# Performance work log

Measured on AMD Instinct MI355X. Metric: run time of the kernel, lower is better.

## Reference

```python
import jax, jax.numpy as jnp
import numpy as np

H = 16  # n_heads
MAX_LEN = 1024


def _skew(x):
    # x: (B, H, N, M) with M == N. Pad 1 column on the left, reshape, drop first row.
    B, h, N, M = x.shape
    x = jnp.pad(x, ((0, 0), (0, 0), (0, 0), (1, 0)))  # (B,H,N,M+1)
    x = x.reshape(B, h, M + 1, N)
    return x[:, :, 1:, :]  # (B,H,N,N)


def setup_inputs() -> dict:
    key = jax.random.key(0)
    ks = jax.random.split(key, 10)
    B, N, C, T = 8, 1024, 1024, 256
    s = 0.02
    return {
        "x": jax.random.normal(ks[0], (B, N, C), dtype=jnp.float32),
        "time_emb": jax.random.normal(ks[1], (B, T), dtype=jnp.float32),
        "W_qkv": jax.random.normal(ks[2], (C, 3 * C), dtype=jnp.float32) * s,
        "b_qkv": jnp.zeros((3 * C,), dtype=jnp.float32),
        "W_time": jax.random.normal(ks[3], (T, 3 * C), dtype=jnp.float32) * s,
        "b_time": jnp.zeros((3 * C,), dtype=jnp.float32),
        "W_out": jax.random.normal(ks[4], (C, C), dtype=jnp.float32) * s,
        "b_out": jnp.zeros((C,), dtype=jnp.float32),
        "Er": jax.random.normal(ks[5], (MAX_LEN, C // H), dtype=jnp.float32) * s,
    }


def reference(x, time_emb, W_qkv, b_qkv, W_time, b_time, W_out, b_out, Er):
    B, N, C = x.shape
    D = C // H
    # token qkv: (B,N,3C) -> (3,B,H,N,D)
    qkv = (x @ W_qkv + b_qkv).reshape(B, N, 3, H, D).transpose(2, 0, 3, 1, 4)
    q, k, v = qkv[0], qkv[1], qkv[2]
    # time qkv: (B,3C) -> (3,B,H,1,D)
    tqkv = (time_emb @ W_time + b_time).reshape(B, 1, 3, H, D).transpose(2, 0, 3, 1, 4)
    q = q + tqkv[0]
    k = k + tqkv[1]
    v = v + tqkv[2]
    # relative position bias
    Er_sl = Er[Er.shape[0] - N:]                      # (N, D)
    rel = jnp.einsum('bhnd,md->bhnm', q, Er_sl)        # (B,H,N,N)
    rel = _skew(rel)
    scale = D ** (-0.5)
    scores = jnp.einsum('bhnd,bhmd->bhnm', q, k) * scale + rel
    attn = jax.nn.softmax(scores, axis=-1)
    out = jnp.einsum('bhnm,bhmd->bhnd', attn, v)       # (B,H,N,D)
    out = out.transpose(0, 2, 1, 3).reshape(B, N, C)
    return out @ W_out + b_out
```

## Files before the change

### kernel.cpp

```cpp
#include <hip/hip_runtime.h>
#include <math.h>

typedef __attribute__((ext_vector_type(8))) short short8;
typedef __attribute__((ext_vector_type(8))) unsigned short ushort8;
typedef __attribute__((ext_vector_type(4))) unsigned short us4;
typedef __attribute__((ext_vector_type(4))) unsigned int u32x4;
typedef __attribute__((ext_vector_type(4))) float f32x4;

#define NH 16
#define HD 64
#define SEQ 1024
#define NB 8
#define CH 1024
#define TD 256
#define GROW 1025
#define LOG2E 1.4426950408889634f

__device__ __forceinline__ unsigned short f2bf(float f) {
  union { float f; unsigned int u; } v; v.f = f;
  unsigned int r = v.u + 0x7FFFu + ((v.u >> 16) & 1u);
  return (unsigned short)(r >> 16);
}
__device__ __forceinline__ float bf2f(unsigned short s) {
  union { unsigned int u; float f; } v; v.u = ((unsigned int)s) << 16;
  return v.f;
}
__device__ __forceinline__ float hexp2(float x) {
  float r;
  asm("v_exp_f32 %0, %1" : "=v"(r) : "v"(x));
  return r;
}
__device__ __forceinline__ void gload_lds16(const unsigned short* g, unsigned short* l) {
  __builtin_amdgcn_global_load_lds(
      (const __attribute__((address_space(1))) unsigned int*)g,
      (__attribute__((address_space(3))) unsigned int*)l, 16, 0, 0);
}

__global__ __launch_bounds__(256) void time_proj_kernel(
    const float* __restrict__ time_emb, const float* __restrict__ W_time,
    const float* __restrict__ b_time, float* __restrict__ tqkv) {
  int idx = blockIdx.x * 256 + threadIdx.x;
  if (idx >= NB * 3072) return;
  int b = idx / 3072, c = idx % 3072;
  float s = b_time[c];
  for (int t = 0; t < TD; ++t) s += time_emb[b * TD + t] * W_time[t * 3072 + c];
  tqkv[idx] = s;
}

__global__ __launch_bounds__(256) void er_convert_kernel(
    const float* __restrict__ Er, unsigned short* __restrict__ Er_bf) {
  int i = blockIdx.x * 256 + threadIdx.x;
  if (i < SEQ * HD) Er_bf[i] = f2bf(Er[i] * LOG2E);
}

__global__ __launch_bounds__(256) void convert_bf_kernel(
    const float* __restrict__ in, unsigned short* __restrict__ out, int n8) {
  int i = blockIdx.x * 256 + threadIdx.x;
  if (i >= n8) return;
  float4 a = ((const float4*)in)[2 * i];
  float4 b = ((const float4*)in)[2 * i + 1];
  ushort8 o;
  o[0] = f2bf(a.x); o[1] = f2bf(a.y); o[2] = f2bf(a.z); o[3] = f2bf(a.w);
  o[4] = f2bf(b.x); o[5] = f2bf(b.y); o[6] = f2bf(b.z); o[7] = f2bf(b.w);
  ((ushort8*)out)[i] = o;
}

__global__ __launch_bounds__(256) void transpose_bf_kernel(
    const float* __restrict__ W, unsigned short* __restrict__ Wt, int R, int Cc) {
  __shared__ float T[64][65];
  int r0 = blockIdx.y * 64, c0 = blockIdx.x * 64;
  for (int idx = threadIdx.x; idx < 4096; idx += 256) {
    int r = idx >> 6, c = idx & 63;
    T[r][c] = W[(size_t)(r0 + r) * Cc + c0 + c];
  }
  __syncthreads();
  for (int idx = threadIdx.x; idx < 4096; idx += 256) {
    int c = idx >> 6, r = idx & 63;
    Wt[(size_t)(c0 + c) * R + r0 + r] = f2bf(T[r][c]);
  }
}

__global__ __launch_bounds__(256) void qkv_gemm_mfma(
    const unsigned short* __restrict__ A, const unsigned short* __restrict__ Bt,
    const float* __restrict__ bqkv, const float* __restrict__ tqkv,
    unsigned short* __restrict__ qb, unsigned short* __restrict__ ksw,
    unsigned short* __restrict__ vtsw) {
  __shared__ unsigned short As[128 * 32];
  __shared__ unsigned short Bs[128 * 32];
  const int m0 = blockIdx.x * 128, n0 = blockIdx.y * 128;
  const int tid = threadIdx.x, l = tid & 63, w = tid >> 6;
  const int wm = w >> 1, wn = w & 1;
  const int grp = l >> 4, col = l & 15;
  f32x4 acc[4][4];
#pragma unroll
  for (int mi = 0; mi < 4; ++mi)
#pragma unroll
    for (int ni = 0; ni < 4; ++ni) acc[mi][ni] = (f32x4){0.f, 0.f, 0.f, 0.f};

  for (int k0 = 0; k0 < 1024; k0 += 32) {
    __syncthreads();
#pragma unroll
    for (int i = 0; i < 2; ++i) {
      int seg = i * 256 + w * 64 + l;
      int mr = seg >> 2, kq = seg & 3;
      gload_lds16(A + (size_t)(m0 + mr) * 1024 + k0 + kq * 8,
                  &As[(i * 256 + w * 64) * 8]);
      gload_lds16(Bt + (size_t)(n0 + mr) * 1024 + k0 + kq * 8,
                  &Bs[(i * 256 + w * 64) * 8]);
    }
    __syncthreads();
    short8 af[4], bfv[4];
#pragma unroll
    for (int mi = 0; mi < 4; ++mi)
      af[mi] = *(const short8*)&As[(wm * 64 + mi * 16 + col) * 32 + grp * 8];
#pragma unroll
    for (int ni = 0; ni < 4; ++ni)
      bfv[ni] = *(const short8*)&Bs[(wn * 64 + ni * 16 + col) * 32 + grp * 8];
#pragma unroll
    for (int mi = 0; mi < 4; ++mi)
#pragma unroll
      for (int ni = 0; ni < 4; ++ni)
        acc[mi][ni] = __builtin_amdgcn_mfma_f32_16x16x32_bf16(af[mi], bfv[ni], acc[mi][ni], 0, 0, 0);
  }

  const int bidx = m0 >> 10;
  const int which = n0 >> 10;
  float biasv[4];
  int hhv[4], dv[4];
#pragma unroll
  for (int ni = 0; ni < 4; ++ni) {
    int c = n0 + wn * 64 + ni * 16 + col;
    biasv[ni] = bqkv[c] + tqkv[bidx * 3072 + c];
    int cc = c & 1023;
    hhv[ni] = cc >> 6;
    dv[ni] = cc & 63;
  }
  if (which == 2) {
    int t = (m0 & 1023) + wm * 64;
#pragma unroll
    for (int ni = 0; ni < 4; ++ni) {
      size_t rowb = ((size_t)(bidx * 16 + hhv[ni]) * 64 + dv[ni]) * 1024;
      int swz = (dv[ni] & 7) << 3;
#pragma unroll
      for (int rr = 0; rr < 4; ++rr) {
        int kbase = (grp * 4 + rr) * 4;
        int colix = t + ((kbase & ~7) ^ swz) + (kbase & 7);
        us4 pk;
#pragma unroll
        for (int mi = 0; mi < 4; ++mi) pk[mi] = f2bf(acc[mi][ni][rr] + biasv[ni]);
        *(us4*)&vtsw[rowb + colix] = pk;
      }
    }
  } else if (which == 1) {
#pragma unroll
    for (int mi = 0; mi < 4; ++mi)
#pragma unroll
      for (int rr = 0; rr < 4; ++rr) {
        int nn = (m0 + wm * 64 + mi * 16 + grp * 4 + rr) & 1023;
#pragma unroll
        for (int ni = 0; ni < 4; ++ni) {
          size_t bhh = (size_t)(bidx * 16 + hhv[ni]);
          ksw[(bhh * 1024 + nn) * 64 + (dv[ni] ^ ((nn & 7) << 3))] =
              f2bf(acc[mi][ni][rr] + biasv[ni]);
        }
      }
  } else {
#pragma unroll
    for (int mi = 0; mi < 4; ++mi)
#pragma unroll
      for (int rr = 0; rr < 4; ++rr) {
        int nn = (m0 + wm * 64 + mi * 16 + grp * 4 + rr) & 1023;
#pragma unroll
        for (int ni = 0; ni < 4; ++ni) {
          size_t bhh = (size_t)(bidx * 16 + hhv[ni]);
          qb[(bhh * 1024 + nn) * 64 + dv[ni]] = f2bf(acc[mi][ni][rr] + biasv[ni]);
        }
      }
  }
}

__global__ __launch_bounds__(256) void out_gemm_mfma(
    const unsigned short* __restrict__ A, const unsigned short* __restrict__ Bt,
    const float* __restrict__ bias, float* __restrict__ out) {
  __shared__ unsigned short As[128 * 32];
  __shared__ unsigned short Bs[128 * 32];
  const int m0 = blockIdx.x * 128, n0 = blockIdx.y * 128;
  const int tid = threadIdx.x, l = tid & 63, w = tid >> 6;
  const int wm = w >> 1, wn = w & 1;
  const int grp = l >> 4, col = l & 15;
  f32x4 acc[4][4];
#pragma unroll
  for (int mi = 0; mi < 4; ++mi)
#pragma unroll
    for (int ni = 0; ni < 4; ++ni) acc[mi][ni] = (f32x4){0.f, 0.f, 0.f, 0.f};

  for (int k0 = 0; k0 < 1024; k0 += 32) {
    __syncthreads();
#pragma unroll
    for (int i = 0; i < 2; ++i) {
      int seg = i * 256 + w * 64 + l;
      int mr = seg >> 2, kq = seg & 3;
      gload_lds16(A + (size_t)(m0 + mr) * 1024 + k0 + kq * 8,
                  &As[(i * 256 + w * 64) * 8]);
      gload_lds16(Bt + (size_t)(n0 + mr) * 1024 + k0 + kq * 8,
                  &Bs[(i * 256 + w * 64) * 8]);
    }
    __syncthreads();
    short8 af[4], bfv[4];
#pragma unroll
    for (int mi = 0; mi < 4; ++mi)
      af[mi] = *(const short8*)&As[(wm * 64 + mi * 16 + col) * 32 + grp * 8];
#pragma unroll
    for (int ni = 0; ni < 4; ++ni)
      bfv[ni] = *(const short8*)&Bs[(wn * 64 + ni * 16 + col) * 32 + grp * 8];
#pragma unroll
    for (int mi = 0; mi < 4; ++mi)
#pragma unroll
      for (int ni = 0; ni < 4; ++ni)
        acc[mi][ni] = __builtin_amdgcn_mfma_f32_16x16x32_bf16(af[mi], bfv[ni], acc[mi][ni], 0, 0, 0);
  }
  float bv[4];
#pragma unroll
  for (int ni = 0; ni < 4; ++ni) bv[ni] = bias[n0 + wn * 64 + ni * 16 + col];
#pragma unroll
  for (int mi = 0; mi < 4; ++mi)
#pragma unroll
    for (int rr = 0; rr < 4; ++rr) {
      int row = m0 + wm * 64 + mi * 16 + grp * 4 + rr;
#pragma unroll
      for (int ni = 0; ni < 4; ++ni) {
        int c = n0 + wn * 64 + ni * 16 + col;
        out[(size_t)row * 1024 + c] = acc[mi][ni][rr] + bv[ni];
      }
    }
}

__global__ __launch_bounds__(256) void g_gemm2(
    const unsigned short* __restrict__ qb, int bh_base,
    const unsigned short* __restrict__ Er_bf,
    unsigned short* __restrict__ Gp) {
  const int n0 = blockIdx.x * 64;
  const int jq = blockIdx.y;
  const int bhl = blockIdx.z;
  const int bh = bh_base + bhl;
  const int tid = threadIdx.x, l = tid & 63, w = tid >> 6;
  const int grp = l >> 4, col = l & 15;
  const int jw = jq * 256 + w * 64;

  short8 aq[4][2];
#pragma unroll
  for (int rf = 0; rf < 4; ++rf)
#pragma unroll
    for (int dc = 0; dc < 2; ++dc)
      aq[rf][dc] = *(const short8*)(qb + ((size_t)bh * SEQ + n0 + rf * 16 + col) * HD + dc * 32 + grp * 8);

  f32x4 acc[4][4];
#pragma unroll
  for (int rf = 0; rf < 4; ++rf)
#pragma unroll
    for (int cf = 0; cf < 4; ++cf) acc[rf][cf] = (f32x4){0.f, 0.f, 0.f, 0.f};

#pragma unroll
  for (int cf = 0; cf < 4; ++cf)
#pragma unroll
    for (int dc = 0; dc < 2; ++dc) {
      short8 bfrag = *(const short8*)(Er_bf + (size_t)(jw + cf * 16 + col) * HD + dc * 32 + grp * 8);
#pragma unroll
      for (int rf = 0; rf < 4; ++rf)
        acc[rf][cf] = __builtin_amdgcn_mfma_f32_16x16x32_bf16(aq[rf][dc], bfrag, acc[rf][cf], 0, 0, 0);
    }

#pragma unroll
  for (int rf = 0; rf < 4; ++rf)
#pragma unroll
    for (int cf = 0; cf < 4; ++cf)
#pragma unroll
      for (int rr = 0; rr < 4; ++rr) {
        int n = n0 + rf * 16 + grp * 4 + rr;
        int j = jw + cf * 16 + col;
        Gp[((size_t)(bhl * SEQ + n)) * GROW + j] = f2bf(acc[rf][cf][rr]);
      }
  if (jq == 3 && tid < 64) {
    int n = n0 + tid;
    Gp[((size_t)(bhl * SEQ + n)) * GROW + 1024] = 0;
  }
}

__global__ __launch_bounds__(256) void attn_kernel(
    const unsigned short* __restrict__ qb, const unsigned short* __restrict__ ksw,
    const unsigned short* __restrict__ vtsw, const unsigned short* __restrict__ Gp,
    unsigned short* __restrict__ attn_o, int bh_base) {
  __shared__ __align__(16) unsigned short KsL[2][4096];
  __shared__ __align__(16) unsigned short VtL[2][4096];
  __shared__ __align__(16) unsigned short Band[2][64][72];
  __shared__ __align__(16) unsigned short Pw[4][16][72];

  const int wg = blockIdx.x + 16 * blockIdx.y;
  const int chunk = 2 * gridDim.y;
  const int nid = (wg & 7) * chunk + (wg >> 3);
  const int bhl = nid >> 4;
  const int n0 = (nid & 15) * 64;
  const int bh = bh_base + bhl;
  const int b = bh >> 4, h = bh & 15;
  const int tid = threadIdx.x, lane = tid & 63, wq = tid >> 6;
  const int grp = lane >> 4, col = lane & 15;
  const int n0w = n0 + wq * 16;

  short8 aq[2];
#pragma unroll
  for (int dc = 0; dc < 2; ++dc)
    aq[dc] = *(const short8*)(qb + ((size_t)(bh * SEQ + n0w + col)) * HD + dc * 32 + grp * 8);

  f32x4 acco[4];
#pragma unroll
  for (int oc = 0; oc < 4; ++oc) acco[oc] = (f32x4){0.f, 0.f, 0.f, 0.f};
  float mrun = -INFINITY, lrun = 0.f;

  const float scale2 = 0.125f * LOG2E;
  const unsigned short* kbh = ksw + (size_t)bh * SEQ * HD;
  const unsigned short* vbh = vtsw + (size_t)bh * HD * SEQ;
  const unsigned short* gbase = Gp + (size_t)(bhl * SEQ + n0) * GROW + (1016 - n0);

  auto STAGE = [&](int buf, int m0) {
#pragma unroll
    for (int i = 0; i < 2; ++i) {
      int gi = i * 256 + wq * 64 + lane;
      int row = gi >> 3, gc = gi & 7;
      gload_lds16(kbh + (((size_t)(m0 + row)) << 6) + gc * 8,
                  &KsL[buf][(i * 256 + wq * 64) * 8]);
      gload_lds16(vbh + (((size_t)row) << 10) + m0 + gc * 8,
                  &VtL[buf][(i * 256 + wq * 64) * 8]);
    }
    const unsigned short* gsrc = gbase + m0;
    unsigned short* bdst = &Band[buf][0][0];
    const int g0 = wq * 144;
#pragma unroll
    for (int it = 0; it < 2; ++it) {
      int g = g0 + it * 64 + lane;
      int r = g / 9, seg = g - r * 9;
      gload_lds16(gsrc + r * 1024 + seg * 8, bdst + g * 8);
    }
    if (lane < 16) {
      int g = g0 + 128 + lane;
      int r = g / 9, seg = g - r * 9;
      gload_lds16(gsrc + r * 1024 + seg * 8, bdst + g * 8);
    }
  };

  STAGE(0, 0);
  __syncthreads();

  for (int t = 0; t < 16; ++t) {
    const int cur = t & 1;
    if (t < 15) STAGE(cur ^ 1, (t + 1) * 64);
    f32x4 acc[4];
#pragma unroll
    for (int mc = 0; mc < 4; ++mc) acc[mc] = (f32x4){0.f, 0.f, 0.f, 0.f};
    __builtin_amdgcn_s_setprio(1);
#pragma unroll
    for (int mc = 0; mc < 4; ++mc)
#pragma unroll
      for (int dc = 0; dc < 2; ++dc) {
        short8 bk = *(const short8*)&KsL[cur][(mc * 16 + col) * 64 + (((dc * 4 + grp) ^ (col & 7)) << 3)];
        acc[mc] = __builtin_amdgcn_mfma_f32_16x16x32_bf16(bk, aq[dc], acc[mc], 0, 0, 0);
      }
    __builtin_amdgcn_s_setprio(0);
    float s[4][4];
    const int dr = wq * 16 + col;
#pragma unroll
    for (int mc = 0; mc < 4; ++mc)
#pragma unroll
      for (int r = 0; r < 4; ++r)
        s[mc][r] = fmaf(acc[mc][r], scale2, bf2f(Band[cur][dr][7 + mc * 16 + grp * 4 + r]));
    float mx = s[0][0];
#pragma unroll
    for (int mc = 0; mc < 4; ++mc)
#pragma unroll
      for (int r = 0; r < 4; ++r) mx = fmaxf(mx, s[mc][r]);
    mx = fmaxf(mx, __shfl_xor(mx, 16));
    mx = fmaxf(mx, __shfl_xor(mx, 32));
    if (mx > mrun) {
      float cr = hexp2(mrun - mx);
      mrun = mx;
      lrun *= cr;
#pragma unroll
      for (int oc = 0; oc < 4; ++oc)
#pragma unroll
        for (int r = 0; r < 4; ++r) acco[oc][r] *= cr;
    }
    float p[4][4];
#pragma unroll
    for (int mc = 0; mc < 4; ++mc)
#pragma unroll
      for (int r = 0; r < 4; ++r) {
        p[mc][r] = hexp2(s[mc][r] - mrun);
        lrun += p[mc][r];
      }
    unsigned int wpk[8];
#pragma unroll
    for (int r = 0; r < 4; ++r)
#pragma unroll
      for (int mh = 0; mh < 2; ++mh)
        asm("v_cvt_pk_bf16_f32 %0, %1, %2"
            : "=v"(wpk[r * 2 + mh]) : "v"(p[mh * 2][r]), "v"(p[mh * 2 + 1][r]));
    *(u32x4*)&Pw[wq][col][grp * 16] = (u32x4){wpk[0], wpk[1], wpk[2], wpk[3]};
    *(u32x4*)&Pw[wq][col][grp * 16 + 8] = (u32x4){wpk[4], wpk[5], wpk[6], wpk[7]};
    short8 ap[2];
#pragma unroll
    for (int kc = 0; kc < 2; ++kc)
      ap[kc] = *(const short8*)&Pw[wq][col][kc * 32 + grp * 8];
    __builtin_amdgcn_s_setprio(1);
#pragma unroll
    for (int oc = 0; oc < 4; ++oc)
#pragma unroll
      for (int kc = 0; kc < 2; ++kc) {
        short8 bv = *(const short8*)&VtL[cur][(oc * 16 + col) * 64 + (((kc * 4 + grp) ^ (col & 7)) << 3)];
        acco[oc] = __builtin_amdgcn_mfma_f32_16x16x32_bf16(bv, ap[kc], acco[oc], 0, 0, 0);
      }
    __builtin_amdgcn_s_setprio(0);
    __syncthreads();
  }
  float tot = lrun;
  tot += __shfl_xor(tot, 16);
  tot += __shfl_xor(tot, 32);
  float inv = 1.0f / tot;
  const int n = n0w + col;
#pragma unroll
  for (int oc = 0; oc < 4; ++oc) {
    us4 pk;
#pragma unroll
    for (int r = 0; r < 4; ++r) pk[r] = f2bf(acco[oc][r] * inv);
    *(us4*)&attn_o[((size_t)(b * SEQ + n)) * CH + h * HD + oc * 16 + grp * 4] = pk;
  }
}

extern "C" void kernel_launch(void* const* d_in, const int* in_sizes, int n_in,
                              void* d_out, int out_size, void* d_ws, size_t ws_size,
                              hipStream_t stream) {
  const float* x        = (const float*)d_in[0];
  const float* time_emb = (const float*)d_in[1];
  const float* W_qkv    = (const float*)d_in[2];
  const float* b_qkv    = (const float*)d_in[3];
  const float* W_time   = (const float*)d_in[4];
  const float* b_time   = (const float*)d_in[5];
  const float* W_out    = (const float*)d_in[6];
  const float* b_out    = (const float*)d_in[7];
  const float* Er       = (const float*)d_in[8];
  float* out = (float*)d_out;

  char* p = (char*)d_ws;
  float* tqkv = (float*)p;                      p += 98304;
  unsigned short* qb = (unsigned short*)p;      p += 16777216;
  unsigned short* ksw = (unsigned short*)p;     p += 16777216;
  unsigned short* vtsw = (unsigned short*)p;    p += 16777216;
  unsigned short* attn_o = (unsigned short*)p;  p += 16777216;
  unsigned short* Er_bf = (unsigned short*)p;   p += 131072;
  unsigned short* Wout_t = (unsigned short*)p;  p += 2097152;
  unsigned short* x_bf = (unsigned short*)p;
  unsigned short* Wqkv_t = x_bf + (size_t)8388608;
  unsigned short* Gp = (unsigned short*)p;

  size_t fixed = (size_t)(p - (char*)d_ws);
  int slab_bh = (ws_size >= fixed + (size_t)64 * 2099200) ? 64 : 32;
  int nslab = 128 / slab_bh;

  er_convert_kernel<<<256, 256, 0, stream>>>(Er, Er_bf);
  time_proj_kernel<<<96, 256, 0, stream>>>(time_emb, W_time, b_time, tqkv);
  convert_bf_kernel<<<4096, 256, 0, stream>>>(x, x_bf, 1048576);
  transpose_bf_kernel<<<dim3(48, 16), 256, 0, stream>>>(W_qkv, Wqkv_t, 1024, 3072);
  transpose_bf_kernel<<<dim3(16, 16), 256, 0, stream>>>(W_out, Wout_t, 1024, 1024);
  qkv_gemm_mfma<<<dim3(64, 24), 256, 0, stream>>>(x_bf, Wqkv_t, b_qkv, tqkv, qb, ksw, vtsw);
  for (int s = 0; s < nslab; ++s) {
    int bh_base = s * slab_bh;
    g_gemm2<<<dim3(16, 4, slab_bh), 256, 0, stream>>>(qb, bh_base, Er_bf, Gp);
    attn_kernel<<<dim3(16, slab_bh), 256, 0, stream>>>(qb, ksw, vtsw, Gp, attn_o, bh_base);
  }
  out_gemm_mfma<<<dim3(64, 8), 256, 0, stream>>>(attn_o, Wout_t, b_out, out);
}
```

Before: 383.9 us.

## Double attention query tile per block and split QKV GEMM into per-output templated launches

The attention kernel now handles 128 query rows per block, with each wave owning two 16-row fragments. Every K/V fragment loaded from LDS therefore feeds two MFMAs, which halves K/V staging traffic per query. The band buffer is now single-buffered at twice the size and is restaged after a mid-iteration barrier. This adds registers and a sync per step and halves the grid size. Separately, the QKV GEMM is split into three template-specialized launches so the Q/K/V epilogue branch is resolved at compile time.

```diff
diff --git a/kernel.cpp b/kernel.cpp
--- a/kernel.cpp
+++ b/kernel.cpp
@@ -80,11 +80,11 @@
   }
 }
 
-__global__ __launch_bounds__(256) void qkv_gemm_mfma(
+template <int WHICH>
+__global__ __launch_bounds__(256) void qkv_gemm_w(
     const unsigned short* __restrict__ A, const unsigned short* __restrict__ Bt,
-    const float* __restrict__ bqkv, const float* __restrict__ tqkv,
-    unsigned short* __restrict__ qb, unsigned short* __restrict__ ksw,
-    unsigned short* __restrict__ vtsw) {
+    const float* __restrict__ bq, const float* __restrict__ tq,
+    unsigned short* __restrict__ dst) {
   __shared__ unsigned short As[128 * 32];
   __shared__ unsigned short Bs[128 * 32];
   const int m0 = blockIdx.x * 128, n0 = blockIdx.y * 128;
@@ -124,18 +124,16 @@
   }
 
   const int bidx = m0 >> 10;
-  const int which = n0 >> 10;
   float biasv[4];
   int hhv[4], dv[4];
 #pragma unroll
   for (int ni = 0; ni < 4; ++ni) {
-    int c = n0 + wn * 64 + ni * 16 + col;
-    biasv[ni] = bqkv[c] + tqkv[bidx * 3072 + c];
-    int cc = c & 1023;
-    hhv[ni] = cc >> 6;
-    dv[ni] = cc & 63;
-  }
-  if (which == 2) {
+    int c2 = n0 + wn * 64 + ni * 16 + col;
+    biasv[ni] = bq[c2] + tq[bidx * 3072 + c2];
+    hhv[ni] = c2 >> 6;
+    dv[ni] = c2 & 63;
+  }
+  if (WHICH == 2) {
     int t = (m0 & 1023) + wm * 64;
 #pragma unroll
     for (int ni = 0; ni < 4; ++ni) {
@@ -148,10 +146,10 @@
         us4 pk;
 #pragma unroll
         for (int mi = 0; mi < 4; ++mi) pk[mi] = f2bf(acc[mi][ni][rr] + biasv[ni]);
-        *(us4*)&vtsw[rowb + colix] = pk;
-      }
-    }
-  } else if (which == 1) {
+        *(us4*)&dst[rowb + colix] = pk;
+      }
+    }
+  } else if (WHICH == 1) {
 #pragma unroll
     for (int mi = 0; mi < 4; ++mi)
 #pragma unroll
@@ -160,7 +158,7 @@
 #pragma unroll
         for (int ni = 0; ni < 4; ++ni) {
           size_t bhh = (size_t)(bidx * 16 + hhv[ni]);
-          ksw[(bhh * 1024 + nn) * 64 + (dv[ni] ^ ((nn & 7) << 3))] =
+          dst[(bhh * 1024 + nn) * 64 + (dv[ni] ^ ((nn & 7) << 3))] =
               f2bf(acc[mi][ni][rr] + biasv[ni]);
         }
       }
@@ -173,7 +171,7 @@
 #pragma unroll
         for (int ni = 0; ni < 4; ++ni) {
           size_t bhh = (size_t)(bidx * 16 + hhv[ni]);
-          qb[(bhh * 1024 + nn) * 64 + dv[ni]] = f2bf(acc[mi][ni][rr] + biasv[ni]);
+          dst[(bhh * 1024 + nn) * 64 + dv[ni]] = f2bf(acc[mi][ni][rr] + biasv[ni]);
         }
       }
   }
@@ -292,36 +290,39 @@
     unsigned short* __restrict__ attn_o, int bh_base) {
   __shared__ __align__(16) unsigned short KsL[2][4096];
   __shared__ __align__(16) unsigned short VtL[2][4096];
-  __shared__ __align__(16) unsigned short Band[2][64][72];
-  __shared__ __align__(16) unsigned short Pw[4][16][72];
-
-  const int wg = blockIdx.x + 16 * blockIdx.y;
-  const int chunk = 2 * gridDim.y;
+  __shared__ __align__(16) unsigned short Band[128][72];
+  __shared__ __align__(16) unsigned short Pw[4][32][72];
+
+  const int wg = blockIdx.x + 8 * blockIdx.y;
+  const int chunk = gridDim.y;
   const int nid = (wg & 7) * chunk + (wg >> 3);
-  const int bhl = nid >> 4;
-  const int n0 = (nid & 15) * 64;
+  const int bhl = nid >> 3;
+  const int n0 = (nid & 7) * 128;
   const int bh = bh_base + bhl;
   const int b = bh >> 4, h = bh & 15;
   const int tid = threadIdx.x, lane = tid & 63, wq = tid >> 6;
   const int grp = lane >> 4, col = lane & 15;
-  const int n0w = n0 + wq * 16;
-
-  short8 aq[2];
-#pragma unroll
-  for (int dc = 0; dc < 2; ++dc)
-    aq[dc] = *(const short8*)(qb + ((size_t)(bh * SEQ + n0w + col)) * HD + dc * 32 + grp * 8);
-
-  f32x4 acco[4];
-#pragma unroll
-  for (int oc = 0; oc < 4; ++oc) acco[oc] = (f32x4){0.f, 0.f, 0.f, 0.f};
-  float mrun = -INFINITY, lrun = 0.f;
+
+  short8 aq[2][2];
+#pragma unroll
+  for (int nf = 0; nf < 2; ++nf)
+#pragma unroll
+    for (int dc = 0; dc < 2; ++dc)
+      aq[nf][dc] = *(const short8*)(qb + ((size_t)(bh * SEQ + n0 + wq * 32 + nf * 16 + col)) * HD + dc * 32 + grp * 8);
+
+  f32x4 acco[2][4];
+#pragma unroll
+  for (int nf = 0; nf < 2; ++nf)
+#pragma unroll
+    for (int oc = 0; oc < 4; ++oc) acco[nf][oc] = (f32x4){0.f, 0.f, 0.f, 0.f};
+  float mrun[2] = {-INFINITY, -INFINITY}, lrun[2] = {0.f, 0.f};
 
   const float scale2 = 0.125f * LOG2E;
   const unsigned short* kbh = ksw + (size_t)bh * SEQ * HD;
   const unsigned short* vbh = vtsw + (size_t)bh * HD * SEQ;
   const unsigned short* gbase = Gp + (size_t)(bhl * SEQ + n0) * GROW + (1016 - n0);
 
-  auto STAGE = [&](int buf, int m0) {
+  auto STAGE_KV = [&](int buf, int m0) {
 #pragma unroll
     for (int i = 0; i < 2; ++i) {
       int gi = i * 256 + wq * 64 + lane;
@@ -331,106 +332,125 @@
       gload_lds16(vbh + (((size_t)row) << 10) + m0 + gc * 8,
                   &VtL[buf][(i * 256 + wq * 64) * 8]);
     }
+  };
+  auto STAGE_BAND = [&](int m0) {
     const unsigned short* gsrc = gbase + m0;
-    unsigned short* bdst = &Band[buf][0][0];
-    const int g0 = wq * 144;
-#pragma unroll
-    for (int it = 0; it < 2; ++it) {
+    unsigned short* bdst = &Band[0][0];
+    const int g0 = wq * 288;
+#pragma unroll
+    for (int it = 0; it < 4; ++it) {
       int g = g0 + it * 64 + lane;
       int r = g / 9, seg = g - r * 9;
       gload_lds16(gsrc + r * 1024 + seg * 8, bdst + g * 8);
     }
-    if (lane < 16) {
-      int g = g0 + 128 + lane;
+    if (lane < 32) {
+      int g = g0 + 256 + lane;
       int r = g / 9, seg = g - r * 9;
       gload_lds16(gsrc + r * 1024 + seg * 8, bdst + g * 8);
     }
   };
 
-  STAGE(0, 0);
+  STAGE_KV(0, 0);
+  STAGE_BAND(0);
   __syncthreads();
 
   for (int t = 0; t < 16; ++t) {
     const int cur = t & 1;
-    if (t < 15) STAGE(cur ^ 1, (t + 1) * 64);
-    f32x4 acc[4];
-#pragma unroll
-    for (int mc = 0; mc < 4; ++mc) acc[mc] = (f32x4){0.f, 0.f, 0.f, 0.f};
+    if (t < 15) STAGE_KV(cur ^ 1, (t + 1) * 64);
+    f32x4 acc[2][4];
+#pragma unroll
+    for (int nf = 0; nf < 2; ++nf)
+#pragma unroll
+      for (int mc = 0; mc < 4; ++mc) acc[nf][mc] = (f32x4){0.f, 0.f, 0.f, 0.f};
     __builtin_amdgcn_s_setprio(1);
 #pragma unroll
     for (int mc = 0; mc < 4; ++mc)
 #pragma unroll
       for (int dc = 0; dc < 2; ++dc) {
         short8 bk = *(const short8*)&KsL[cur][(mc * 16 + col) * 64 + (((dc * 4 + grp) ^ (col & 7)) << 3)];
-        acc[mc] = __builtin_amdgcn_mfma_f32_16x16x32_bf16(bk, aq[dc], acc[mc], 0, 0, 0);
+#pragma unroll
+        for (int nf = 0; nf < 2; ++nf)
+          acc[nf][mc] = __builtin_amdgcn_mfma_f32_16x16x32_bf16(bk, aq[nf][dc], acc[nf][mc], 0, 0, 0);
       }
     __builtin_amdgcn_s_setprio(0);
-    float s[4][4];
-    const int dr = wq * 16 + col;
-#pragma unroll
-    for (int mc = 0; mc < 4; ++mc)
+#pragma unroll
+    for (int nf = 0; nf < 2; ++nf) {
+      const int dr = wq * 32 + nf * 16 + col;
+      float s[4][4];
+#pragma unroll
+      for (int mc = 0; mc < 4; ++mc)
+#pragma unroll
+        for (int r = 0; r < 4; ++r)
+          s[mc][r] = fmaf(acc[nf][mc][r], scale2, bf2f(Band[dr][7 + mc * 16 + grp * 4 + r]));
+      float mx = s[0][0];
+#pragma unroll
+      for (int mc = 0; mc < 4; ++mc)
+#pragma unroll
+        for (int r = 0; r < 4; ++r) mx = fmaxf(mx, s[mc][r]);
+      mx = fmaxf(mx, __shfl_xor(mx, 16));
+      mx = fmaxf(mx, __shfl_xor(mx, 32));
+      if (mx > mrun[nf]) {
+        float cr = hexp2(mrun[nf] - mx);
+        mrun[nf] = mx;
+        lrun[nf] *= cr;
+#pragma unroll
+        for (int oc = 0; oc < 4; ++oc)
+#pragma unroll
+          for (int r = 0; r < 4; ++r) acco[nf][oc][r] *= cr;
+      }
+      float p[4][4];
+#pragma unroll
+      for (int mc = 0; mc < 4; ++mc)
+#pragma unroll
+        for (int r = 0; r < 4; ++r) {
+          p[mc][r] = hexp2(s[mc][r] - mrun[nf]);
+          lrun[nf] += p[mc][r];
+        }
+      unsigned int wpk[8];
 #pragma unroll
       for (int r = 0; r < 4; ++r)
-        s[mc][r] = fmaf(acc[mc][r], scale2, bf2f(Band[cur][dr][7 + mc * 16 + grp * 4 + r]));
-    float mx = s[0][0];
-#pragma unroll
-    for (int mc = 0; mc < 4; ++mc)
-#pragma unroll
-      for (int r = 0; r < 4; ++r) mx = fmaxf(mx, s[mc][r]);
-    mx = fmaxf(mx, __shfl_xor(mx, 16));
-    mx = fmaxf(mx, __shfl_xor(mx, 32));
-    if (mx > mrun) {
-      float cr = hexp2(mrun - mx);
-      mrun = mx;
-      lrun *= cr;
-#pragma unroll
-      for (int oc = 0; oc < 4; ++oc)
-#pragma unroll
-        for (int r = 0; r < 4; ++r) acco[oc][r] *= cr;
-    }
-    float p[4][4];
-#pragma unroll
-    for (int mc = 0; mc < 4; ++mc)
-#pragma unroll
-      for (int r = 0; r < 4; ++r) {
-        p[mc][r] = hexp2(s[mc][r] - mrun);
-        lrun += p[mc][r];
-      }
-    unsigned int wpk[8];
-#pragma unroll
-    for (int r = 0; r < 4; ++r)
-#pragma unroll
-      for (int mh = 0; mh < 2; ++mh)
-        asm("v_cvt_pk_bf16_f32 %0, %1, %2"
-            : "=v"(wpk[r * 2 + mh]) : "v"(p[mh * 2][r]), "v"(p[mh * 2 + 1][r]));
-    *(u32x4*)&Pw[wq][col][grp * 16] = (u32x4){wpk[0], wpk[1], wpk[2], wpk[3]};
-    *(u32x4*)&Pw[wq][col][grp * 16 + 8] = (u32x4){wpk[4], wpk[5], wpk[6], wpk[7]};
-    short8 ap[2];
-#pragma unroll
-    for (int kc = 0; kc < 2; ++kc)
-      ap[kc] = *(const short8*)&Pw[wq][col][kc * 32 + grp * 8];
+#pragma unroll
+        for (int mh = 0; mh < 2; ++mh)
+          asm("v_cvt_pk_bf16_f32 %0, %1, %2"
+              : "=v"(wpk[r * 2 + mh]) : "v"(p[mh * 2][r]), "v"(p[mh * 2 + 1][r]));
+      *(u32x4*)&Pw[wq][nf * 16 + col][grp * 16] = (u32x4){wpk[0], wpk[1], wpk[2], wpk[3]};
+      *(u32x4*)&Pw[wq][nf * 16 + col][grp * 16 + 8] = (u32x4){wpk[4], wpk[5], wpk[6], wpk[7]};
+    }
+    __syncthreads();
+    if (t < 15) STAGE_BAND((t + 1) * 64);
+    short8 ap[2][2];
+#pragma unroll
+    for (int nf = 0; nf < 2; ++nf)
+#pragma unroll
+      for (int kc = 0; kc < 2; ++kc)
+        ap[nf][kc] = *(const short8*)&Pw[wq][nf * 16 + col][kc * 32 + grp * 8];
     __builtin_amdgcn_s_setprio(1);
 #pragma unroll
     for (int oc = 0; oc < 4; ++oc)
 #pragma unroll
       for (int kc = 0; kc < 2; ++kc) {
         short8 bv = *(const short8*)&VtL[cur][(oc * 16 + col) * 64 + (((kc * 4 + grp) ^ (col & 7)) << 3)];
-        acco[oc] = __builtin_amdgcn_mfma_f32_16x16x32_bf16(bv, ap[kc], acco[oc], 0, 0, 0);
+#pragma unroll
+        for (int nf = 0; nf < 2; ++nf)
+          acco[nf][oc] = __builtin_amdgcn_mfma_f32_16x16x32_bf16(bv, ap[nf][kc], acco[nf][oc], 0, 0, 0);
       }
     __builtin_amdgcn_s_setprio(0);
     __syncthreads();
   }
-  float tot = lrun;
-  tot += __shfl_xor(tot, 16);
-  tot += __shfl_xor(tot, 32);
-  float inv = 1.0f / tot;
-  const int n = n0w + col;
-#pragma unroll
-  for (int oc = 0; oc < 4; ++oc) {
-    us4 pk;
-#pragma unroll
-    for (int r = 0; r < 4; ++r) pk[r] = f2bf(acco[oc][r] * inv);
-    *(us4*)&attn_o[((size_t)(b * SEQ + n)) * CH + h * HD + oc * 16 + grp * 4] = pk;
+#pragma unroll
+  for (int nf = 0; nf < 2; ++nf) {
+    float tot = lrun[nf];
+    tot += __shfl_xor(tot, 16);
+    tot += __shfl_xor(tot, 32);
+    float inv = 1.0f / tot;
+    const int n = n0 + wq * 32 + nf * 16 + col;
+#pragma unroll
+    for (int oc = 0; oc < 4; ++oc) {
+      us4 pk;
+#pragma unroll
+      for (int r = 0; r < 4; ++r) pk[r] = f2bf(acco[nf][oc][r] * inv);
+      *(us4*)&attn_o[((size_t)(b * SEQ + n)) * CH + h * HD + oc * 16 + grp * 4] = pk;
+    }
   }
 }
 
@@ -469,11 +489,15 @@
   convert_bf_kernel<<<4096, 256, 0, stream>>>(x, x_bf, 1048576);
   transpose_bf_kernel<<<dim3(48, 16), 256, 0, stream>>>(W_qkv, Wqkv_t, 1024, 3072);
   transpose_bf_kernel<<<dim3(16, 16), 256, 0, stream>>>(W_out, Wout_t, 1024, 1024);
-  qkv_gemm_mfma<<<dim3(64, 24), 256, 0, stream>>>(x_bf, Wqkv_t, b_qkv, tqkv, qb, ksw, vtsw);
+  qkv_gemm_w<0><<<dim3(64, 8), 256, 0, stream>>>(x_bf, Wqkv_t, b_qkv, tqkv, qb);
+  qkv_gemm_w<1><<<dim3(64, 8), 256, 0, stream>>>(x_bf, Wqkv_t + (size_t)1048576,
+                                                 b_qkv + 1024, tqkv + 1024, ksw);
+  qkv_gemm_w<2><<<dim3(64, 8), 256, 0, stream>>>(x_bf, Wqkv_t + (size_t)2097152,
+                                                 b_qkv + 2048, tqkv + 2048, vtsw);
   for (int s = 0; s < nslab; ++s) {
     int bh_base = s * slab_bh;
     g_gemm2<<<dim3(16, 4, slab_bh), 256, 0, stream>>>(qb, bh_base, Er_bf, Gp);
-    attn_kernel<<<dim3(16, slab_bh), 256, 0, stream>>>(qb, ksw, vtsw, Gp, attn_o, bh_base);
+    attn_kernel<<<dim3(8, slab_bh), 256, 0, stream>>>(qb, ksw, vtsw, Gp, attn_o, bh_base);
   }
   out_gemm_mfma<<<dim3(64, 8), 256, 0, stream>>>(attn_o, Wout_t, b_out, out);
 }
```

New measurement: 367.2 us. 1.05x faster.
